# Optimization experiments

Measured on AMD Instinct MI355X. Metric: run time of the kernel, lower is better.

The kernel has to match this reference:

```python
import jax, jax.numpy as jnp
import numpy as np

B, L = 4, 512
V, D, NL = 16384, 384, 8
DS, DC, EXP = 16, 4, 2
DI = D * EXP            # 768
DTR = (D + 15) // 16    # dt_rank = 24
ED = 256


def setup_inputs() -> dict:
    key = jax.random.key(0)
    ks = jax.random.split(key, 12)
    s = lambda k, shape, scale=0.02: jax.random.normal(k, shape, jnp.float32) * scale
    input_ids = jax.random.randint(ks[0], (B, L), 0, V)
    emb = s(ks[1], (V, D)).at[0].set(0.0)          # padding_idx=0 row is zero
    pos_emb = s(ks[2], (512, D))
    ln_g = jnp.ones((NL, D)); ln_b = jnp.zeros((NL, D))
    in_proj_w = s(ks[3], (NL, 2 * DI, D))
    conv_w = s(ks[4], (NL, DI, DC), 0.1)
    conv_b = jnp.zeros((NL, DI))
    x_proj_w = s(ks[5], (NL, DTR + 2 * DS, DI))
    dt_proj_w = s(ks[6], (NL, DI, DTR), 0.1)
    dt_proj_b = jnp.full((NL, DI), -4.0) + s(ks[7], (NL, DI), 0.1)
    # official Mamba S4D-real init: A_log = log(1..d_state)
    A_log = jnp.broadcast_to(jnp.log(jnp.arange(1.0, DS + 1.0, dtype=jnp.float32)), (NL, DI, DS))
    D_param = jnp.ones((NL, DI))
    out_proj_w = s(ks[8], (NL, D, DI))
    fln_g = jnp.ones((D,)); fln_b = jnp.zeros((D,))
    proj_w = s(ks[9], (ED, D)); proj_b = jnp.zeros((ED,))
    return {"input_ids": input_ids, "emb": emb, "pos_emb": pos_emb, "ln_g": ln_g, "ln_b": ln_b,
            "in_proj_w": in_proj_w, "conv_w": conv_w, "conv_b": conv_b, "x_proj_w": x_proj_w,
            "dt_proj_w": dt_proj_w, "dt_proj_b": dt_proj_b, "A_log": A_log, "D_param": D_param,
            "out_proj_w": out_proj_w, "fln_g": fln_g, "fln_b": fln_b, "proj_w": proj_w, "proj_b": proj_b}


def layernorm(x, g, b):
    m = jnp.mean(x, -1, keepdims=True)
    v = jnp.mean(jnp.square(x - m), -1, keepdims=True)
    return (x - m) * jax.lax.rsqrt(v + 1e-5) * g + b


def mamba_block(x, in_w, cw, cb, xw, dtw, dtb, Alog, Dp, ow):
    # x: (B, L, D)
    b, l, _ = x.shape
    xz = jnp.einsum('bld,ed->ble', x, in_w)              # (B, L, 2*DI)
    xc, z = jnp.split(xz, 2, axis=-1)
    # causal depthwise conv1d, kernel DC
    xp = jnp.pad(xc, ((0, 0), (DC - 1, 0), (0, 0)))
    xconv = cb + sum(xp[:, k:k + l, :] * cw[:, k] for k in range(DC))
    xconv = jax.nn.silu(xconv)                            # (B, L, DI)
    dbc = jnp.einsum('bld,ed->ble', xconv, xw)            # (B, L, DTR+2*DS)
    dt_r = dbc[..., :DTR]
    Bs = dbc[..., DTR:DTR + DS]                           # (B, L, DS)
    Cs = dbc[..., DTR + DS:]                              # (B, L, DS)
    dt = jax.nn.softplus(jnp.einsum('blr,dr->bld', dt_r, dtw) + dtb)  # (B, L, DI)
    A = -jnp.exp(Alog)                                    # (DI, DS)
    dA = jnp.exp(dt[..., None] * A)                       # (B, L, DI, DS)
    dBu = dt[..., None] * Bs[:, :, None, :] * xconv[..., None]

    def step(h, inp):
        a, bu, c = inp
        h = a * h + bu                                    # (B, DI, DS)
        return h, jnp.einsum('bdn,bn->bd', h, c)

    h0 = jnp.zeros((b, DI, DS), x.dtype)
    _, ys = jax.lax.scan(step, h0, (dA.transpose(1, 0, 2, 3), dBu.transpose(1, 0, 2, 3), Cs.transpose(1, 0, 2)))
    y = ys.transpose(1, 0, 2) + Dp * xconv                # (B, L, DI)
    y = y * jax.nn.silu(z)
    return jnp.einsum('bld,od->blo', y, ow)               # (B, L, D)


def reference(input_ids, emb, pos_emb, ln_g, ln_b, in_proj_w, conv_w, conv_b, x_proj_w,
              dt_proj_w, dt_proj_b, A_log, D_param, out_proj_w, fln_g, fln_b, proj_w, proj_b):
    _, l = input_ids.shape
    x = emb[input_ids] + pos_emb[:l]
    for i in range(NL):
        x = x + mamba_block(layernorm(x, ln_g[i], ln_b[i]), in_proj_w[i], conv_w[i], conv_b[i],
                            x_proj_w[i], dt_proj_w[i], dt_proj_b[i], A_log[i], D_param[i], out_proj_w[i])
    x = layernorm(x, fln_g, fln_b)
    mask = (input_ids != 0)[..., None].astype(x.dtype)
    pooled = (x * mask).sum(1) / jnp.clip(mask.sum(1), 1.0)
    e = pooled @ proj_w.T + proj_b
    return e / jnp.maximum(jnp.linalg.norm(e, axis=-1, keepdims=True), 1e-12)
```

## Files before the change

kernel.cpp:

```cpp
#include <hip/hip_runtime.h>
#include <hip/hip_bf16.h>
#include <math.h>

#define B 4
#define L 512
#define D 384
#define NL 8
#define DS 16
#define DC 4
#define DI 768
#define DTR 24
#define G (DTR + 2*DS)
#define ED 256
#define M (B*L)
#define NCH 32
#define CHL (L/NCH)

typedef __attribute__((ext_vector_type(8))) short short8;
typedef __attribute__((ext_vector_type(4))) float f32x4;
typedef unsigned short ushort_t;

__device__ inline unsigned bf2(float a, float b) {
  unsigned ua = __float_as_uint(a), ub = __float_as_uint(b);
  ua = (ua + 0x7FFFu + ((ua >> 16) & 1u)) >> 16;
  ub = (ub + 0x7FFFu + ((ub >> 16) & 1u)) >> 16;
  return (ua & 0xFFFFu) | (ub << 16);
}
__device__ inline ushort_t bf1(float a) {
  unsigned u = __float_as_uint(a);
  u = (u + 0x7FFFu + ((u >> 16) & 1u)) >> 16;
  return (ushort_t)u;
}

__global__ __launch_bounds__(256) void f2bf_kernel(const float* __restrict__ in,
    ushort_t* __restrict__ out, int n8) {
  int i = blockIdx.x * 256 + threadIdx.x;
  if (i >= n8) return;
  float4 a = *(const float4*)(in + (size_t)i * 8);
  float4 b = *(const float4*)(in + (size_t)i * 8 + 4);
  *(uint4*)(out + (size_t)i * 8) =
      make_uint4(bf2(a.x, a.y), bf2(a.z, a.w), bf2(b.x, b.y), bf2(b.z, b.w));
}

__global__ __launch_bounds__(256) void embed_kernel(const int* __restrict__ ids,
    const float* __restrict__ emb, const float* __restrict__ pos, float* __restrict__ x) {
  int idx = blockIdx.x * 256 + threadIdx.x;
  if (idx >= M * D) return;
  int m = idx / D, d = idx - m * D;
  int l = m & (L - 1);
  x[idx] = emb[(size_t)ids[m] * D + d] + pos[l * D + d];
}

__global__ __launch_bounds__(64) void layernorm_kernel(const float* __restrict__ x,
    const float* __restrict__ g, const float* __restrict__ b,
    float* __restrict__ o, ushort_t* __restrict__ obf) {
  int row = blockIdx.x;
  int t = threadIdx.x;
  const float* xr = x + (size_t)row * D;
  float v[6];
  float s = 0.f;
#pragma unroll
  for (int i = 0; i < 6; i++) { v[i] = xr[t + i * 64]; s += v[i]; }
#pragma unroll
  for (int o_ = 32; o_ > 0; o_ >>= 1) s += __shfl_xor(s, o_);
  float mean = s * (1.0f / D);
  float vs = 0.f;
#pragma unroll
  for (int i = 0; i < 6; i++) { float dd = v[i] - mean; vs += dd * dd; }
#pragma unroll
  for (int o_ = 32; o_ > 0; o_ >>= 1) vs += __shfl_xor(vs, o_);
  float inv = 1.0f / sqrtf(vs * (1.0f / D) + 1e-5f);
  float* orow = o + (size_t)row * D;
  ushort_t* brow = obf + (size_t)row * D;
#pragma unroll
  for (int i = 0; i < 6; i++) {
    int d = t + i * 64;
    float val = (v[i] - mean) * inv * g[d] + b[d];
    orow[d] = val;
    brow[d] = bf1(val);
  }
}

template <int ADD>
__global__ __launch_bounds__(128) void gemm_bt_kernel(const ushort_t* __restrict__ A,
    const ushort_t* __restrict__ W, float* __restrict__ C, int Mm, int Nn, int Kk) {
  __shared__ uint4 As[32 * 8];
  __shared__ uint4 Bs[64 * 8];
  int t = threadIdx.x;
  int lane = t & 63, w = t >> 6;
  int m0 = blockIdx.x * 32, n0 = blockIdx.y * 64;

  f32x4 acc[2][2] = {};

  for (int k0 = 0; k0 < Kk; k0 += 64) {
    uint4 av[2], bv[4];
#pragma unroll
    for (int u = 0; u < 2; u++) {
      int q = t + u * 128;
      int row = q >> 3, p = q & 7;
      av[u] = *(const uint4*)(A + (size_t)(m0 + row) * Kk + k0 + ((p ^ (row & 7)) << 3));
    }
#pragma unroll
    for (int u = 0; u < 4; u++) {
      int q = t + u * 128;
      int row = q >> 3, p = q & 7;
      int grow = n0 + row;
      if (grow < Nn)
        bv[u] = *(const uint4*)(W + (size_t)grow * Kk + k0 + ((p ^ (row & 7)) << 3));
      else
        bv[u] = make_uint4(0u, 0u, 0u, 0u);
    }
    __syncthreads();
#pragma unroll
    for (int u = 0; u < 2; u++) As[t + u * 128] = av[u];
#pragma unroll
    for (int u = 0; u < 4; u++) Bs[t + u * 128] = bv[u];
    __syncthreads();
#pragma unroll
    for (int kk = 0; kk < 2; kk++) {
      int ks = kk * 4 + (lane >> 4);
      short8 af[2], bfv[2];
#pragma unroll
      for (int i = 0; i < 2; i++) {
        int ra = i * 16 + (lane & 15);
        af[i] = *(short8*)&As[ra * 8 + (ks ^ (ra & 7))];
      }
#pragma unroll
      for (int j = 0; j < 2; j++) {
        int rb = w * 32 + j * 16 + (lane & 15);
        bfv[j] = *(short8*)&Bs[rb * 8 + (ks ^ (rb & 7))];
      }
#pragma unroll
      for (int i = 0; i < 2; i++)
#pragma unroll
        for (int j = 0; j < 2; j++)
          acc[i][j] = __builtin_amdgcn_mfma_f32_16x16x32_bf16(af[i], bfv[j], acc[i][j], 0, 0, 0);
    }
  }

#pragma unroll
  for (int i = 0; i < 2; i++) {
    int cm = m0 + i * 16 + (lane >> 4) * 4;
#pragma unroll
    for (int j = 0; j < 2; j++) {
      int cn = n0 + w * 32 + j * 16 + (lane & 15);
      if (cn >= Nn) continue;
#pragma unroll
      for (int r = 0; r < 4; r++) {
        size_t off = (size_t)(cm + r) * Nn + cn;
        float v = acc[i][j][r];
        if (ADD) v += C[off];
        C[off] = v;
      }
    }
  }
}

__global__ __launch_bounds__(256) void conv_silu_kernel(const float* __restrict__ xz,
    const float* __restrict__ cw, const float* __restrict__ cb,
    float* __restrict__ xc, ushort_t* __restrict__ xcbf) {
  int idx = blockIdx.x * 256 + threadIdx.x;
  if (idx >= M * DI) return;
  int m = idx / DI, e = idx - m * DI;
  int l = m & (L - 1);
  float acc = cb[e];
#pragma unroll
  for (int k = 0; k < DC; k++) {
    int ll = l - (DC - 1) + k;
    if (ll >= 0) acc += xz[(size_t)(m - (DC - 1) + k) * (2 * DI) + e] * cw[e * DC + k];
  }
  float sv = acc / (1.f + __expf(-acc));
  xc[idx] = sv;
  xcbf[idx] = bf1(sv);
}

__global__ __launch_bounds__(256) void dt_kernel(const float* __restrict__ dbc,
    const float* __restrict__ dtw, const float* __restrict__ dtb, float* __restrict__ dt) {
  int tok = blockIdx.x;
  __shared__ float rr[DTR];
  int t = threadIdx.x;
  if (t < DTR) rr[t] = dbc[(size_t)tok * G + t];
  __syncthreads();
  for (int d = t; d < DI; d += 256) {
    float acc = dtb[d];
#pragma unroll
    for (int k = 0; k < DTR; k++) acc += rr[k] * dtw[d * DTR + k];
    dt[(size_t)tok * DI + d] = (acc > 20.f) ? acc : log1pf(expf(acc));
  }
}

__global__ __launch_bounds__(64) void scan_pass1(const float* __restrict__ dbc,
    const float* __restrict__ dt, const float* __restrict__ xconv,
    const float* __restrict__ A_log, float* __restrict__ Aprod, float* __restrict__ Sloc) {
  int bc = blockIdx.x;
  int b = bc >> 5, c = bc & (NCH - 1);
  int d = blockIdx.y * 64 + threadIdx.x;
  float Av[DS], h[DS], ap[DS];
#pragma unroll
  for (int n = 0; n < DS; n++) {
    Av[n] = -__expf(A_log[d * DS + n]);
    h[n] = 0.f; ap[n] = 1.f;
  }
  size_t tok0 = (size_t)b * L + c * CHL;
  for (int l = 0; l < CHL; l++) {
    size_t tok = tok0 + l;
    float dtv = dt[tok * DI + d];
    float xcv = xconv[tok * DI + d];
    const float4* Bp = (const float4*)(dbc + tok * G + DTR);
    float dbx = dtv * xcv;
#pragma unroll
    for (int q = 0; q < 4; q++) {
      float4 B4 = Bp[q];
      float dA;
      dA = __expf(dtv * Av[q*4+0]); ap[q*4+0] *= dA; h[q*4+0] = dA * h[q*4+0] + dbx * B4.x;
      dA = __expf(dtv * Av[q*4+1]); ap[q*4+1] *= dA; h[q*4+1] = dA * h[q*4+1] + dbx * B4.y;
      dA = __expf(dtv * Av[q*4+2]); ap[q*4+2] *= dA; h[q*4+2] = dA * h[q*4+2] + dbx * B4.z;
      dA = __expf(dtv * Av[q*4+3]); ap[q*4+3] *= dA; h[q*4+3] = dA * h[q*4+3] + dbx * B4.w;
    }
  }
  float* Ap = Aprod + ((size_t)bc * DI + d) * DS;
  float* Sp = Sloc  + ((size_t)bc * DI + d) * DS;
#pragma unroll
  for (int q = 0; q < 4; q++) {
    *(float4*)(Ap + q * 4) = make_float4(ap[q*4+0], ap[q*4+1], ap[q*4+2], ap[q*4+3]);
    *(float4*)(Sp + q * 4) = make_float4(h[q*4+0], h[q*4+1], h[q*4+2], h[q*4+3]);
  }
}

__global__ __launch_bounds__(256) void scan_pass2(const float* __restrict__ Aprod,
    float* __restrict__ Sloc) {
  int idx = blockIdx.x * 256 + threadIdx.x;
  int b = idx / (DI * DS);
  int dn = idx - b * DI * DS;
  float h = 0.f;
#pragma unroll
  for (int c = 0; c < NCH; c++) {
    size_t o = (size_t)(b * NCH + c) * DI * DS + dn;
    float a = Aprod[o];
    float s = Sloc[o];
    Sloc[o] = h;
    h = a * h + s;
  }
}

__global__ __launch_bounds__(64) void scan_pass3(const float* __restrict__ dbc,
    const float* __restrict__ dt, const float* __restrict__ xconv,
    const float* __restrict__ xz, const float* __restrict__ A_log,
    const float* __restrict__ Dp, const float* __restrict__ Sloc,
    ushort_t* __restrict__ y) {
  int bc = blockIdx.x;
  int b = bc >> 5, c = bc & (NCH - 1);
  int d = blockIdx.y * 64 + threadIdx.x;
  float Av[DS], h[DS];
  const float* Hs = Sloc + ((size_t)bc * DI + d) * DS;
#pragma unroll
  for (int n = 0; n < DS; n++) {
    Av[n] = -__expf(A_log[d * DS + n]);
    h[n] = Hs[n];
  }
  float Dv = Dp[d];
  size_t tok0 = (size_t)b * L + c * CHL;
  for (int l = 0; l < CHL; l++) {
    size_t tok = tok0 + l;
    float dtv = dt[tok * DI + d];
    float xcv = xconv[tok * DI + d];
    float zv = xz[tok * (2 * DI) + DI + d];
    const float4* BC = (const float4*)(dbc + tok * G + DTR);
    float dbx = dtv * xcv;
    float p = 0.f;
#pragma unroll
    for (int q = 0; q < 4; q++) {
      float4 B4 = BC[q];
      float4 C4 = BC[q + 4];
      float dA;
      dA = __expf(dtv * Av[q*4+0]); h[q*4+0] = dA * h[q*4+0] + dbx * B4.x; p += h[q*4+0] * C4.x;
      dA = __expf(dtv * Av[q*4+1]); h[q*4+1] = dA * h[q*4+1] + dbx * B4.y; p += h[q*4+1] * C4.y;
      dA = __expf(dtv * Av[q*4+2]); h[q*4+2] = dA * h[q*4+2] + dbx * B4.z; p += h[q*4+2] * C4.z;
      dA = __expf(dtv * Av[q*4+3]); h[q*4+3] = dA * h[q*4+3] + dbx * B4.w; p += h[q*4+3] * C4.w;
    }
    float yv = (p + Dv * xcv) * (zv / (1.f + __expf(-zv)));
    y[tok * DI + d] = bf1(yv);
  }
}

__global__ __launch_bounds__(128) void pool_kernel(const float* __restrict__ xf,
    const int* __restrict__ ids, float* __restrict__ pooled) {
  int b = blockIdx.x;
  int t = threadIdx.x;
  float cnt = 0.f;
  float sums[3] = {};
  for (int l = 0; l < L; l++) {
    int tok = b * L + l;
    float msk = (ids[tok] != 0) ? 1.f : 0.f;
    cnt += msk;
#pragma unroll
    for (int i = 0; i < 3; i++) sums[i] += msk * xf[(size_t)tok * D + t + i * 128];
  }
  float denom = fmaxf(cnt, 1.f);
#pragma unroll
  for (int i = 0; i < 3; i++) pooled[b * D + t + i * 128] = sums[i] / denom;
}

__global__ __launch_bounds__(256) void proj_norm_kernel(const float* __restrict__ pooled,
    const float* __restrict__ pw, const float* __restrict__ pb, float* __restrict__ out) {
  int b = blockIdx.x;
  int t = threadIdx.x;
  __shared__ float pr[D];
  __shared__ float red[256];
  for (int i = t; i < D; i += 256) pr[i] = pooled[b * D + i];
  __syncthreads();
  float acc = pb[t];
  for (int k = 0; k < D; k++) acc += pr[k] * pw[t * D + k];
  red[t] = acc * acc;
  __syncthreads();
  for (int s = 128; s > 0; s >>= 1) {
    if (t < s) red[t] += red[t + s];
    __syncthreads();
  }
  float nrm = sqrtf(red[0]);
  float scale = 1.f / fmaxf(nrm, 1e-12f);
  out[b * ED + t] = acc * scale;
}

extern "C" void kernel_launch(void* const* d_in, const int* in_sizes, int n_in,
                              void* d_out, int out_size, void* d_ws, size_t ws_size,
                              hipStream_t stream) {
  const int*   ids  = (const int*)d_in[0];
  const float* emb  = (const float*)d_in[1];
  const float* pos  = (const float*)d_in[2];
  const float* ln_g = (const float*)d_in[3];
  const float* ln_b = (const float*)d_in[4];
  const float* inw  = (const float*)d_in[5];
  const float* cw   = (const float*)d_in[6];
  const float* cb   = (const float*)d_in[7];
  const float* xw   = (const float*)d_in[8];
  const float* dtw  = (const float*)d_in[9];
  const float* dtb  = (const float*)d_in[10];
  const float* Alog = (const float*)d_in[11];
  const float* Dp   = (const float*)d_in[12];
  const float* ow   = (const float*)d_in[13];
  const float* flng = (const float*)d_in[14];
  const float* flnb = (const float*)d_in[15];
  const float* pw   = (const float*)d_in[16];
  const float* pb   = (const float*)d_in[17];
  float* out = (float*)d_out;

  float* ws    = (float*)d_ws;
  float* x      = ws;
  float* xln    = x + (size_t)M * D;
  float* xz     = xln + (size_t)M * D;
  float* xconv  = xz + (size_t)M * 2 * DI;
  float* dbc    = xconv + (size_t)M * DI;
  float* dtb_   = dbc + (size_t)M * G;
  float* pooled = dtb_ + (size_t)M * DI;
  ushort_t* bfbase   = (ushort_t*)(pooled + (size_t)B * D);
  ushort_t* xln_bf   = bfbase;
  ushort_t* xconv_bf = xln_bf + (size_t)M * D;
  ushort_t* ybuf_bf  = xconv_bf + (size_t)M * DI;
  ushort_t* inw_bf   = ybuf_bf + (size_t)M * DI;
  ushort_t* xw_bf    = inw_bf + (size_t)NL * 2 * DI * D;
  ushort_t* ow_bf    = xw_bf + (size_t)NL * G * DI;
  float* Aprod = (float*)(ow_bf + (size_t)NL * D * DI);
  float* Sloc  = Aprod + (size_t)B * NCH * DI * DS;

  {
    int n8;
    n8 = NL * 2 * DI * D / 8;
    f2bf_kernel<<<(n8 + 255) / 256, 256, 0, stream>>>(inw, inw_bf, n8);
    n8 = NL * G * DI / 8;
    f2bf_kernel<<<(n8 + 255) / 256, 256, 0, stream>>>(xw, xw_bf, n8);
    n8 = NL * D * DI / 8;
    f2bf_kernel<<<(n8 + 255) / 256, 256, 0, stream>>>(ow, ow_bf, n8);
  }

  embed_kernel<<<(M * D + 255) / 256, 256, 0, stream>>>(ids, emb, pos, x);

  for (int i = 0; i < NL; i++) {
    layernorm_kernel<<<M, 64, 0, stream>>>(x, ln_g + i * D, ln_b + i * D, xln, xln_bf);

    dim3 g1(M / 32, (2 * DI) / 64);
    gemm_bt_kernel<0><<<g1, 128, 0, stream>>>(xln_bf, inw_bf + (size_t)i * 2 * DI * D, xz, M, 2 * DI, D);

    conv_silu_kernel<<<(M * DI + 255) / 256, 256, 0, stream>>>(
        xz, cw + (size_t)i * DI * DC, cb + (size_t)i * DI, xconv, xconv_bf);

    dim3 g2(M / 32, (G + 63) / 64);
    gemm_bt_kernel<0><<<g2, 128, 0, stream>>>(xconv_bf, xw_bf + (size_t)i * G * DI, dbc, M, G, DI);

    dt_kernel<<<M, 256, 0, stream>>>(dbc, dtw + (size_t)i * DI * DTR, dtb + (size_t)i * DI, dtb_);

    dim3 gs(B * NCH, DI / 64);
    scan_pass1<<<gs, 64, 0, stream>>>(dbc, dtb_, xconv,
        Alog + (size_t)i * DI * DS, Aprod, Sloc);
    scan_pass2<<<(B * DI * DS) / 256, 256, 0, stream>>>(Aprod, Sloc);
    scan_pass3<<<gs, 64, 0, stream>>>(dbc, dtb_, xconv, xz,
        Alog + (size_t)i * DI * DS, Dp + (size_t)i * DI, Sloc, ybuf_bf);

    dim3 g3(M / 32, D / 64);
    gemm_bt_kernel<1><<<g3, 128, 0, stream>>>(ybuf_bf, ow_bf + (size_t)i * D * DI, x, M, D, DI);
  }

  layernorm_kernel<<<M, 64, 0, stream>>>(x, flng, flnb, xln, xln_bf);
  pool_kernel<<<B, 128, 0, stream>>>(xln, ids, pooled);
  proj_norm_kernel<<<B, ED, 0, stream>>>(pooled, pw, pb, out);
}
```

Measured before the change: 1.052 ms.

## Fuse dt projection into scan passes, merge weight casts, parallelize pooling

Removes the separate dt_kernel and its M×DI dt buffer. Both scan passes now compute the softplus dt projection inline from the dbc row, using per-thread registers holding the dt weights. The three bf16 weight-conversion launches are merged into one kernel, and the final mean pooling is split into a 16-way partial reduction plus a final combine for more parallelism. These changes trade extra recomputation of the 24-term dot product (done twice, in pass1 and pass3) and more register pressure for less memory traffic and fewer launches.

```diff
diff --git a/kernel.cpp b/kernel.cpp
--- a/kernel.cpp
+++ b/kernel.cpp
@@ -32,14 +32,20 @@
   return (ushort_t)u;
 }
 
-__global__ __launch_bounds__(256) void f2bf_kernel(const float* __restrict__ in,
-    ushort_t* __restrict__ out, int n8) {
+__global__ __launch_bounds__(256) void f2bf3_kernel(
+    const float* __restrict__ a, ushort_t* __restrict__ oa, int na8,
+    const float* __restrict__ b, ushort_t* __restrict__ ob, int nb8,
+    const float* __restrict__ c, ushort_t* __restrict__ oc, int nc8) {
   int i = blockIdx.x * 256 + threadIdx.x;
-  if (i >= n8) return;
-  float4 a = *(const float4*)(in + (size_t)i * 8);
-  float4 b = *(const float4*)(in + (size_t)i * 8 + 4);
-  *(uint4*)(out + (size_t)i * 8) =
-      make_uint4(bf2(a.x, a.y), bf2(a.z, a.w), bf2(b.x, b.y), bf2(b.z, b.w));
+  const float* in; ushort_t* out; int j;
+  if (i < na8) { in = a; out = oa; j = i; }
+  else if (i < na8 + nb8) { in = b; out = ob; j = i - na8; }
+  else if (i < na8 + nb8 + nc8) { in = c; out = oc; j = i - na8 - nb8; }
+  else return;
+  float4 p = *(const float4*)(in + (size_t)j * 8);
+  float4 q = *(const float4*)(in + (size_t)j * 8 + 4);
+  *(uint4*)(out + (size_t)j * 8) =
+      make_uint4(bf2(p.x, p.y), bf2(p.z, p.w), bf2(q.x, q.y), bf2(q.z, q.w));
 }
 
 __global__ __launch_bounds__(256) void embed_kernel(const int* __restrict__ ids,
@@ -174,27 +180,18 @@
   xcbf[idx] = bf1(sv);
 }
 
-__global__ __launch_bounds__(256) void dt_kernel(const float* __restrict__ dbc,
-    const float* __restrict__ dtw, const float* __restrict__ dtb, float* __restrict__ dt) {
-  int tok = blockIdx.x;
-  __shared__ float rr[DTR];
-  int t = threadIdx.x;
-  if (t < DTR) rr[t] = dbc[(size_t)tok * G + t];
-  __syncthreads();
-  for (int d = t; d < DI; d += 256) {
-    float acc = dtb[d];
-#pragma unroll
-    for (int k = 0; k < DTR; k++) acc += rr[k] * dtw[d * DTR + k];
-    dt[(size_t)tok * DI + d] = (acc > 20.f) ? acc : log1pf(expf(acc));
-  }
-}
-
 __global__ __launch_bounds__(64) void scan_pass1(const float* __restrict__ dbc,
-    const float* __restrict__ dt, const float* __restrict__ xconv,
-    const float* __restrict__ A_log, float* __restrict__ Aprod, float* __restrict__ Sloc) {
+    const float* __restrict__ xconv, const float* __restrict__ A_log,
+    const float* __restrict__ dtw, const float* __restrict__ dtb,
+    float* __restrict__ Aprod, float* __restrict__ Sloc) {
   int bc = blockIdx.x;
   int b = bc >> 5, c = bc & (NCH - 1);
   int d = blockIdx.y * 64 + threadIdx.x;
+  float Wd[DTR];
+#pragma unroll
+  for (int q = 0; q < 6; q++)
+    *(float4*)&Wd[q * 4] = *(const float4*)(dtw + (size_t)d * DTR + q * 4);
+  float dtbv = dtb[d];
   float Av[DS], h[DS], ap[DS];
 #pragma unroll
   for (int n = 0; n < DS; n++) {
@@ -204,9 +201,16 @@
   size_t tok0 = (size_t)b * L + c * CHL;
   for (int l = 0; l < CHL; l++) {
     size_t tok = tok0 + l;
-    float dtv = dt[tok * DI + d];
+    const float* row = dbc + tok * G;
+    float r_[DTR];
+#pragma unroll
+    for (int q = 0; q < 6; q++) *(float4*)&r_[q * 4] = *(const float4*)(row + q * 4);
+    float sp = dtbv;
+#pragma unroll
+    for (int k = 0; k < DTR; k++) sp += r_[k] * Wd[k];
+    float dtv = (sp > 20.f) ? sp : log1pf(__expf(sp));
     float xcv = xconv[tok * DI + d];
-    const float4* Bp = (const float4*)(dbc + tok * G + DTR);
+    const float4* Bp = (const float4*)(row + DTR);
     float dbx = dtv * xcv;
 #pragma unroll
     for (int q = 0; q < 4; q++) {
@@ -244,13 +248,18 @@
 }
 
 __global__ __launch_bounds__(64) void scan_pass3(const float* __restrict__ dbc,
-    const float* __restrict__ dt, const float* __restrict__ xconv,
-    const float* __restrict__ xz, const float* __restrict__ A_log,
-    const float* __restrict__ Dp, const float* __restrict__ Sloc,
-    ushort_t* __restrict__ y) {
+    const float* __restrict__ xconv, const float* __restrict__ xz,
+    const float* __restrict__ A_log, const float* __restrict__ dtw,
+    const float* __restrict__ dtb, const float* __restrict__ Dp,
+    const float* __restrict__ Sloc, ushort_t* __restrict__ y) {
   int bc = blockIdx.x;
   int b = bc >> 5, c = bc & (NCH - 1);
   int d = blockIdx.y * 64 + threadIdx.x;
+  float Wd[DTR];
+#pragma unroll
+  for (int q = 0; q < 6; q++)
+    *(float4*)&Wd[q * 4] = *(const float4*)(dtw + (size_t)d * DTR + q * 4);
+  float dtbv = dtb[d];
   float Av[DS], h[DS];
   const float* Hs = Sloc + ((size_t)bc * DI + d) * DS;
 #pragma unroll
@@ -262,10 +271,17 @@
   size_t tok0 = (size_t)b * L + c * CHL;
   for (int l = 0; l < CHL; l++) {
     size_t tok = tok0 + l;
-    float dtv = dt[tok * DI + d];
+    const float* row = dbc + tok * G;
+    float r_[DTR];
+#pragma unroll
+    for (int q = 0; q < 6; q++) *(float4*)&r_[q * 4] = *(const float4*)(row + q * 4);
+    float sp = dtbv;
+#pragma unroll
+    for (int k = 0; k < DTR; k++) sp += r_[k] * Wd[k];
+    float dtv = (sp > 20.f) ? sp : log1pf(__expf(sp));
     float xcv = xconv[tok * DI + d];
     float zv = xz[tok * (2 * DI) + DI + d];
-    const float4* BC = (const float4*)(dbc + tok * G + DTR);
+    const float4* BC = (const float4*)(row + DTR);
     float dbx = dtv * xcv;
     float p = 0.f;
 #pragma unroll
@@ -283,22 +299,38 @@
   }
 }
 
-__global__ __launch_bounds__(128) void pool_kernel(const float* __restrict__ xf,
-    const int* __restrict__ ids, float* __restrict__ pooled) {
+__global__ __launch_bounds__(128) void pool_partial(const float* __restrict__ xf,
+    const int* __restrict__ ids, float* __restrict__ psum, float* __restrict__ pcnt) {
+  int b = blockIdx.x, g = blockIdx.y;
+  int t = threadIdx.x;
+  float cnt = 0.f;
+  float sums[3] = {};
+  for (int l = g * 32; l < g * 32 + 32; l++) {
+    int tok = b * L + l;
+    float msk = (ids[tok] != 0) ? 1.f : 0.f;
+    cnt += msk;
+#pragma unroll
+    for (int i = 0; i < 3; i++) sums[i] += msk * xf[(size_t)tok * D + t + i * 128];
+  }
+#pragma unroll
+  for (int i = 0; i < 3; i++) psum[(size_t)(b * 16 + g) * D + t + i * 128] = sums[i];
+  if (t == 0) pcnt[b * 16 + g] = cnt;
+}
+
+__global__ __launch_bounds__(128) void pool_final(const float* __restrict__ psum,
+    const float* __restrict__ pcnt, float* __restrict__ pooled) {
   int b = blockIdx.x;
   int t = threadIdx.x;
   float cnt = 0.f;
-  float sums[3] = {};
-  for (int l = 0; l < L; l++) {
-    int tok = b * L + l;
-    float msk = (ids[tok] != 0) ? 1.f : 0.f;
-    cnt += msk;
-#pragma unroll
-    for (int i = 0; i < 3; i++) sums[i] += msk * xf[(size_t)tok * D + t + i * 128];
+  float s[3] = {};
+  for (int g = 0; g < 16; g++) {
+    cnt += pcnt[b * 16 + g];
+#pragma unroll
+    for (int i = 0; i < 3; i++) s[i] += psum[(size_t)(b * 16 + g) * D + t + i * 128];
   }
   float denom = fmaxf(cnt, 1.f);
 #pragma unroll
-  for (int i = 0; i < 3; i++) pooled[b * D + t + i * 128] = sums[i] / denom;
+  for (int i = 0; i < 3; i++) pooled[b * D + t + i * 128] = s[i] / denom;
 }
 
 __global__ __launch_bounds__(256) void proj_norm_kernel(const float* __restrict__ pooled,
@@ -351,8 +383,7 @@
   float* xz     = xln + (size_t)M * D;
   float* xconv  = xz + (size_t)M * 2 * DI;
   float* dbc    = xconv + (size_t)M * DI;
-  float* dtb_   = dbc + (size_t)M * G;
-  float* pooled = dtb_ + (size_t)M * DI;
+  float* pooled = dbc + (size_t)M * G;
   ushort_t* bfbase   = (ushort_t*)(pooled + (size_t)B * D);
   ushort_t* xln_bf   = bfbase;
   ushort_t* xconv_bf = xln_bf + (size_t)M * D;
@@ -362,15 +393,16 @@
   ushort_t* ow_bf    = xw_bf + (size_t)NL * G * DI;
   float* Aprod = (float*)(ow_bf + (size_t)NL * D * DI);
   float* Sloc  = Aprod + (size_t)B * NCH * DI * DS;
+  float* psum  = Sloc + (size_t)B * NCH * DI * DS;
+  float* pcnt  = psum + (size_t)B * 16 * D;
 
   {
-    int n8;
-    n8 = NL * 2 * DI * D / 8;
-    f2bf_kernel<<<(n8 + 255) / 256, 256, 0, stream>>>(inw, inw_bf, n8);
-    n8 = NL * G * DI / 8;
-    f2bf_kernel<<<(n8 + 255) / 256, 256, 0, stream>>>(xw, xw_bf, n8);
-    n8 = NL * D * DI / 8;
-    f2bf_kernel<<<(n8 + 255) / 256, 256, 0, stream>>>(ow, ow_bf, n8);
+    int na8 = NL * 2 * DI * D / 8;
+    int nb8 = NL * G * DI / 8;
+    int nc8 = NL * D * DI / 8;
+    int tot = na8 + nb8 + nc8;
+    f2bf3_kernel<<<(tot + 255) / 256, 256, 0, stream>>>(
+        inw, inw_bf, na8, xw, xw_bf, nb8, ow, ow_bf, nc8);
   }
 
   embed_kernel<<<(M * D + 255) / 256, 256, 0, stream>>>(ids, emb, pos, x);
@@ -387,20 +419,22 @@
     dim3 g2(M / 32, (G + 63) / 64);
     gemm_bt_kernel<0><<<g2, 128, 0, stream>>>(xconv_bf, xw_bf + (size_t)i * G * DI, dbc, M, G, DI);
 
-    dt_kernel<<<M, 256, 0, stream>>>(dbc, dtw + (size_t)i * DI * DTR, dtb + (size_t)i * DI, dtb_);
-
     dim3 gs(B * NCH, DI / 64);
-    scan_pass1<<<gs, 64, 0, stream>>>(dbc, dtb_, xconv,
-        Alog + (size_t)i * DI * DS, Aprod, Sloc);
+    scan_pass1<<<gs, 64, 0, stream>>>(dbc, xconv,
+        Alog + (size_t)i * DI * DS, dtw + (size_t)i * DI * DTR, dtb + (size_t)i * DI,
+        Aprod, Sloc);
     scan_pass2<<<(B * DI * DS) / 256, 256, 0, stream>>>(Aprod, Sloc);
-    scan_pass3<<<gs, 64, 0, stream>>>(dbc, dtb_, xconv, xz,
-        Alog + (size_t)i * DI * DS, Dp + (size_t)i * DI, Sloc, ybuf_bf);
+    scan_pass3<<<gs, 64, 0, stream>>>(dbc, xconv, xz,
+        Alog + (size_t)i * DI * DS, dtw + (size_t)i * DI * DTR, dtb + (size_t)i * DI,
+        Dp + (size_t)i * DI, Sloc, ybuf_bf);
 
     dim3 g3(M / 32, D / 64);
     gemm_bt_kernel<1><<<g3, 128, 0, stream>>>(ybuf_bf, ow_bf + (size_t)i * D * DI, x, M, D, DI);
   }
 
   layernorm_kernel<<<M, 64, 0, stream>>>(x, flng, flnb, xln, xln_bf);
-  pool_kernel<<<B, 128, 0, stream>>>(xln, ids, pooled);
+  dim3 gp(B, 16);
+  pool_partial<<<gp, 128, 0, stream>>>(xln, ids, psum, pcnt);
+  pool_final<<<B, 128, 0, stream>>>(psum, pcnt, pooled);
   proj_norm_kernel<<<B, ED, 0, stream>>>(pooled, pw, pb, out);
 }
```

Result: faster. 1.021 ms (-2.9%).
